# Kernel optimization log

Measured on AMD Instinct MI355X. Metric: run time of the kernel, lower is better.

## Reference

```python
import jax, jax.numpy as jnp
import numpy as np

T_Q, T_K, B, H, V = 32, 48, 64, 1024, 32320
MASK_FILL = -65504.0  # GNMT uses fp16 min


def setup_inputs() -> dict:
    key = jax.random.key(0)
    ks = jax.random.split(key, 12)
    s = 0.02
    inp = {
        "input1": jax.random.normal(ks[0], (T_K, B, H), jnp.float32),
        "input0": jax.random.normal(ks[1], (T_K, B, H), jnp.float32),
        "input2": jax.random.randint(ks[2], (B,), 1, T_K + 1),          # context lengths in [1, T_K]
        "input3": jax.random.randint(ks[3], (T_Q, B), 0, V),            # decoder token ids
        "emb": (jax.random.normal(ks[4], (V, H), jnp.float32) * 0.1).at[0].set(0.0),  # padding_idx=0
        "W_ih": jax.random.normal(ks[5], (4 * H, H), jnp.float32) * s,
        "W_hh": jax.random.normal(ks[6], (4 * H, H), jnp.float32) * s,
        "b_ih": jnp.zeros((4 * H,), jnp.float32),
        "b_hh": jnp.zeros((4 * H,), jnp.float32),
        "W_q": jax.random.normal(ks[7], (H, H), jnp.float32) * s,
        "W_k": jax.random.normal(ks[8], (H, H), jnp.float32) * s,
        "v_att": jax.random.normal(ks[9], (H,), jnp.float32) * s,
        "norm_scalar": jnp.array([1.0 / np.sqrt(H)], jnp.float32),
        "norm_bias": jnp.zeros((H,), jnp.float32),
    }
    return inp


def _lstm(x, W_ih, W_hh, b_ih, b_hh):
    # x: (T, B, In). PyTorch LSTM gate order: i, f, g, o. Zero initial state.
    xp = jnp.einsum('tbi,gi->tbg', x, W_ih) + b_ih + b_hh  # (T, B, 4H)
    Hh = W_hh.shape[1]

    def step(carry, xt):
        h, c = carry
        gates = xt + h @ W_hh.T
        i, f, g, o = jnp.split(gates, 4, axis=-1)
        c = jax.nn.sigmoid(f) * c + jax.nn.sigmoid(i) * jnp.tanh(g)
        h = jax.nn.sigmoid(o) * jnp.tanh(c)
        return (h, c), h

    h0 = jnp.zeros((x.shape[1], Hh), x.dtype)
    _, hs = jax.lax.scan(step, (h0, h0), xp)
    return hs  # (T, B, H)


def _forward(input1, input0, input2, input3, emb, W_ih, W_hh, b_ih, b_hh,
             W_q, W_k, v_att, norm_scalar, norm_bias):
    x = emb[input3]                       # (T_Q, B, H) embedding lookup
    ctx = input0 + input1                 # (T_K, B, H) residual-summed encoder context
    rnn_out = _lstm(x, W_ih, W_hh, b_ih, b_hh)   # (T_Q, B, H)

    # Bahdanau attention (batch_first=False -> transpose to batch-first)
    q = rnn_out.transpose(1, 0, 2)        # (B, T_Q, H)
    keys = ctx.transpose(1, 0, 2)         # (B, T_K, H)
    aq = q @ W_q.T                        # (B, T_Q, H)
    ak = keys @ W_k.T                     # (B, T_K, H)
    v = v_att / jnp.linalg.norm(v_att) * norm_scalar[0]  # normalized attention vector
    sum_qk = aq[:, :, None, :] + ak[:, None, :, :] + norm_bias  # (B, T_Q, T_K, H)
    scores = jnp.einsum('bqkh,h->bqk', jnp.tanh(sum_qk), v)
    pad = jnp.arange(T_K)[None, :] >= input2[:, None]            # (B, T_K), True = pad
    scores = jnp.where(pad[:, None, :], MASK_FILL, scores)
    attn = jax.nn.softmax(scores, axis=-1)
    context = jnp.einsum('bqk,bkh->bqh', attn, keys).transpose(1, 0, 2)  # (T_Q, B, H)
    # dropout p=0 -> identity; returns (rnn_outputs, attn_context) = (out12, out11)
    return rnn_out, context


def reference(input1, input0, input2, input3, emb, W_ih, W_hh, b_ih, b_hh,
              W_q, W_k, v_att, norm_scalar, norm_bias):
    return _forward(input1, input0, input2, input3, emb, W_ih, W_hh, b_ih, b_hh,
                    W_q, W_k, v_att, norm_scalar, norm_bias)
```

## Files before the change

kernel.cpp:

```cpp
#include <hip/hip_runtime.h>
#include <hip/hip_bf16.h>

typedef unsigned short u16;
typedef __attribute__((ext_vector_type(8))) short bf16x8;
typedef __attribute__((ext_vector_type(8))) unsigned short us8;
typedef __attribute__((ext_vector_type(4))) float f32x4;

#define T_Q 32
#define T_K 48
#define NB 64
#define HDIM 1024
#define MASK_FILL -65504.0f
#define LSTM_BLOCKS 64

__device__ __forceinline__ float bf2f(u16 v){
  union { unsigned u; float f; } x; x.u = ((unsigned)v) << 16; return x.f;
}
__device__ __forceinline__ u16 f2bf(float f){
  union { float f; unsigned u; } x; x.f = f;
  return (u16)((x.u + 0x7FFFu + ((x.u >> 16) & 1u)) >> 16);
}
__device__ __forceinline__ float sigm(float x){
  return __builtin_amdgcn_rcpf(1.f + __expf(-x));
}
__device__ __forceinline__ float tanh_f(float x){
  float e = __expf(2.f * x);
  return fmaf(-2.f, __builtin_amdgcn_rcpf(e + 1.f), 1.f);
}

__device__ __forceinline__ void st_b32_cc(u16* a, unsigned v){
  asm volatile("global_store_dword %0, %1, off sc0 sc1" :: "v"(a), "v"(v) : "memory");
}
__device__ __forceinline__ void st_flag(int* a, int v){
  asm volatile("global_store_dword %0, %1, off sc0 sc1" :: "v"(a), "v"(v) : "memory");
}
__device__ __forceinline__ int ld_flag(const int* a){
  int r;
  asm volatile("global_load_dword %0, %1, off sc0 sc1\n\ts_waitcnt vmcnt(0)"
               : "=v"(r) : "v"(a) : "memory");
  return r;
}

#define MFMA16(A,B,C) __builtin_amdgcn_mfma_f32_16x16x32_bf16(A,B,C,0,0,0)


__global__ void conv_f2b(const float* __restrict__ s, u16* __restrict__ d){
  size_t i = ((size_t)blockIdx.x * 256 + threadIdx.x) * 4;
  float4 v = *(const float4*)(s + i);
  ushort4 o; o.x = f2bf(v.x); o.y = f2bf(v.y); o.z = f2bf(v.z); o.w = f2bf(v.w);
  *(ushort4*)(d + i) = o;
}

__global__ void gather_x(const int* __restrict__ tok, const float* __restrict__ emb,
                         u16* __restrict__ x){
  int r = blockIdx.x;
  int token = tok[r];
  float4 v = ((const float4*)(emb + (size_t)token * HDIM))[threadIdx.x];
  ushort4 o; o.x = f2bf(v.x); o.y = f2bf(v.y); o.z = f2bf(v.z); o.w = f2bf(v.w);
  ((ushort4*)(x + (size_t)r * HDIM))[threadIdx.x] = o;
}

__global__ void make_keys(const float* __restrict__ a, const float* __restrict__ b,
                          u16* __restrict__ o){
  size_t i = ((size_t)blockIdx.x * 256 + threadIdx.x) * 4;
  float4 va = *(const float4*)(a + i);
  float4 vb = *(const float4*)(b + i);
  ushort4 vo;
  vo.x = f2bf(va.x + vb.x);
  vo.y = f2bf(va.y + vb.y);
  vo.z = f2bf(va.z + vb.z);
  vo.w = f2bf(va.w + vb.w);
  *(ushort4*)(o + i) = vo;
}

__global__ void prep_small(const float* __restrict__ vatt, const float* __restrict__ ns,
                           const float* __restrict__ nb,
                           float* __restrict__ vhat, float* __restrict__ nbias){
  __shared__ float wred[4];
  int t = threadIdx.x, lane = t & 63, w = t >> 6;
  float vv[4]; float s = 0.f;
  #pragma unroll
  for (int j = 0; j < 4; j++){ vv[j] = vatt[t*4 + j]; s += vv[j]*vv[j]; }
  #pragma unroll
  for (int m = 32; m >= 1; m >>= 1) s += __shfl_xor(s, m);
  if (lane == 0) wred[w] = s;
  __syncthreads();
  float tot = wred[0] + wred[1] + wred[2] + wred[3];
  float scale = ns[0] / sqrtf(tot);
  #pragma unroll
  for (int j = 0; j < 4; j++) vhat[t*4 + j] = vv[j] * scale;
  #pragma unroll
  for (int j = 0; j < 4; j++){ int i = t + 256*j; nbias[i] = nb[i]; }
}

__global__ void prep_bsum(const float* __restrict__ bih, const float* __restrict__ bhh,
                          float* __restrict__ bias_sum){
  int i = blockIdx.x * 256 + threadIdx.x;
  bias_sum[i] = bih[i] + bhh[i];
}


template<int OB>
__global__ __launch_bounds__(256) void gemm_bf16(
  const u16* __restrict__ A, const u16* __restrict__ W,
  const float* __restrict__ bias, void* __restrict__ Cv,
  int M, int N, int K)
{
  __shared__ __align__(16) u16 As[4][66][8];
  __shared__ __align__(16) u16 Bs[4][66][8];
  const int t = threadIdx.x;
  const int m0 = blockIdx.y * 64, n0 = blockIdx.x * 64;
  const int lane = t & 63, w = t >> 6;
  const int wm = (w >> 1) * 32, wn = (w & 1) * 32;
  const int lr = lane & 15, g = lane >> 4;
  const int lrow = t >> 2, lkc = t & 3;
  f32x4 acc00 = {0,0,0,0}, acc01 = {0,0,0,0}, acc10 = {0,0,0,0}, acc11 = {0,0,0,0};
  const u16* aptr = A + (size_t)(m0 + lrow) * K + lkc * 8;
  const u16* wptr = W + (size_t)(n0 + lrow) * K + lkc * 8;
  for (int k0 = 0; k0 < K; k0 += 32){
    *(bf16x8*)(&As[lkc][lrow][0]) = *(const bf16x8*)(aptr + k0);
    *(bf16x8*)(&Bs[lkc][lrow][0]) = *(const bf16x8*)(wptr + k0);
    __syncthreads();
    bf16x8 a0 = *(const bf16x8*)(&As[g][wm      + lr][0]);
    bf16x8 a1 = *(const bf16x8*)(&As[g][wm + 16 + lr][0]);
    bf16x8 b0 = *(const bf16x8*)(&Bs[g][wn      + lr][0]);
    bf16x8 b1 = *(const bf16x8*)(&Bs[g][wn + 16 + lr][0]);
    acc00 = MFMA16(a0, b0, acc00);
    acc01 = MFMA16(a0, b1, acc01);
    acc10 = MFMA16(a1, b0, acc10);
    acc11 = MFMA16(a1, b1, acc11);
    __syncthreads();
  }
  const int rb = m0 + wm + g * 4;
  const int cb = n0 + wn + lr;
  float bv0 = bias ? bias[cb]      : 0.f;
  float bv1 = bias ? bias[cb + 16] : 0.f;
  #pragma unroll
  for (int r = 0; r < 4; r++){
    float v00 = acc00[r] + bv0, v01 = acc01[r] + bv1;
    float v10 = acc10[r] + bv0, v11 = acc11[r] + bv1;
    if (OB){
      u16* C = (u16*)Cv;
      C[(size_t)(rb + r)      * N + cb]      = f2bf(v00);
      C[(size_t)(rb + r)      * N + cb + 16] = f2bf(v01);
      C[(size_t)(rb + 16 + r) * N + cb]      = f2bf(v10);
      C[(size_t)(rb + 16 + r) * N + cb + 16] = f2bf(v11);
    } else {
      float* C = (float*)Cv;
      C[(size_t)(rb + r)      * N + cb]      = v00;
      C[(size_t)(rb + r)      * N + cb + 16] = v01;
      C[(size_t)(rb + 16 + r) * N + cb]      = v10;
      C[(size_t)(rb + 16 + r) * N + cb + 16] = v11;
    }
  }
}


__global__ __launch_bounds__(512, 1) void lstm_persistent(
  const float* __restrict__ Whh, const u16* __restrict__ xp,
  u16* __restrict__ hsteps,
  u16* __restrict__ qbuf, float* __restrict__ out0,
  int* __restrict__ flags)
{
  extern __shared__ char smem[];
  u16*  wlds = (u16*)smem;
  float* gl  = (float*)(smem + 131072);
  volatile int* lds_ready = (volatile int*)(smem + 147456);

  const int tid = threadIdx.x;
  const int c0 = blockIdx.x * 16;
  const int lane = tid & 63, w = tid >> 6;
  const int gate = w & 3, msub = w >> 2;
  const int lr = lane & 15, g = lane >> 4;

  if (tid < 8) lds_ready[tid] = 0;

  #pragma unroll
  for (int i = 0; i < 16; i++){
    int e = (i * 512 + tid) * 8;
    int R = e >> 10, k = e & 1023;
    int gg = R >> 4, rr = R & 15, tt = k >> 5, kk = k & 31;
    const float* src = Whh + (size_t)((gg << 10) + c0 + rr) * 1024 + k;
    float4 v0 = *(const float4*)(src);
    float4 v1 = *(const float4*)(src + 4);
    u16* dst = wlds + (((gg * 32 + tt) * 16 + rr) * 32 + kk);
    ushort4 o0, o1;
    o0.x = f2bf(v0.x); o0.y = f2bf(v0.y); o0.z = f2bf(v0.z); o0.w = f2bf(v0.w);
    o1.x = f2bf(v1.x); o1.y = f2bf(v1.y); o1.z = f2bf(v1.z); o1.w = f2bf(v1.w);
    *(ushort4*)dst = o0; *(ushort4*)(dst + 4) = o1;
  }
  __syncthreads();

  const int pb = (tid * 2) >> 4;
  const int pc = (tid * 2) & 15;
  float c_state0 = 0.f, c_state1 = 0.f;

  const int arow = msub * 32 + lr;
  const int jc = g >> 1;
  const int cc = (g & 1) * 8;

#define SPING(gq) \
  do { while (lds_ready[gq] < step) __builtin_amdgcn_s_sleep(1); \
       asm volatile("" ::: "memory"); } while (0)

#define LOADG(s0, s1, gq) \
  do { const u16* A0_ = pa0 + (gq) * 8192; const u16* A1_ = pa1 + (gq) * 8192; \
       s0[0] = *(const bf16x8*)(A0_);        s1[0] = *(const bf16x8*)(A1_); \
       s0[1] = *(const bf16x8*)(A0_ + 2048); s1[1] = *(const bf16x8*)(A1_ + 2048); \
       s0[2] = *(const bf16x8*)(A0_ + 4096); s1[2] = *(const bf16x8*)(A1_ + 4096); \
       s0[3] = *(const bf16x8*)(A0_ + 6144); s1[3] = *(const bf16x8*)(A1_ + 6144); } while (0)

#define MFMAG(s0, s1, gq) \
  do { const u16* wb_ = wlds + ((size_t)(gate * 32 + (gq) * 4) * 16 + lr) * 32 + g * 8; \
       bf16x8 b0_ = *(const bf16x8*)(wb_); \
       bf16x8 b1_ = *(const bf16x8*)(wb_ + 512); \
       bf16x8 b2_ = *(const bf16x8*)(wb_ + 1024); \
       bf16x8 b3_ = *(const bf16x8*)(wb_ + 1536); \
       acc0 = MFMA16(s0[0], b0_, acc0); acc1 = MFMA16(s1[0], b0_, acc1); \
       acc0 = MFMA16(s0[1], b1_, acc0); acc1 = MFMA16(s1[1], b1_, acc1); \
       acc0 = MFMA16(s0[2], b2_, acc0); acc1 = MFMA16(s1[2], b2_, acc1); \
       acc0 = MFMA16(s0[3], b3_, acc0); acc1 = MFMA16(s1[3], b3_, acc1); } while (0)

  #pragma unroll 1
  for (int step = 0; step < T_Q; step++){
    const u16* xr = xp + ((size_t)(step * NB + pb)) * 4096 + c0 + pc;
    unsigned xw0 = *(const unsigned*)(xr);
    unsigned xw1 = *(const unsigned*)(xr + 1024);
    unsigned xw2 = *(const unsigned*)(xr + 2048);
    unsigned xw3 = *(const unsigned*)(xr + 3072);

    f32x4 acc0 = {0,0,0,0}, acc1 = {0,0,0,0};

    if (step > 0){
      if (w == 0){
        unsigned done = 0;
        const int* fp = flags + lane * 16;
        while (done != 0xFFu){
          int f = ld_flag(fp);
          unsigned long long b = __ballot(f >= step);
          #pragma unroll
          for (int gq = 0; gq < 8; gq++){
            if (((done >> gq) & 1u) == 0 &&
                ((unsigned)(b >> (gq * 8)) & 0xFFu) == 0xFFu){
              if (lane == 0) lds_ready[gq] = step;
              done |= 1u << gq;
            }
          }
          if (done != 0xFFu) __builtin_amdgcn_s_sleep(1);
        }
      }

      const u16* hb  = hsteps + (size_t)(step - 1) * 65536;
      const u16* pa0 = hb + (size_t)jc * 1024 + (size_t)arow * 16 + cc;
      const u16* pa1 = pa0 + 256;

      bf16x8 sA0[4], sA1[4], sB0[4], sB1[4];
      SPING(0); LOADG(sA0, sA1, 0);
      SPING(1); LOADG(sB0, sB1, 1); MFMAG(sA0, sA1, 0);
      SPING(2); LOADG(sA0, sA1, 2); MFMAG(sB0, sB1, 1);
      SPING(3); LOADG(sB0, sB1, 3); MFMAG(sA0, sA1, 2);
      SPING(4); LOADG(sA0, sA1, 4); MFMAG(sB0, sB1, 3);
      SPING(5); LOADG(sB0, sB1, 5); MFMAG(sA0, sA1, 4);
      SPING(6); LOADG(sA0, sA1, 6); MFMAG(sB0, sB1, 5);
      SPING(7); LOADG(sB0, sB1, 7); MFMAG(sA0, sA1, 6);
      MFMAG(sB0, sB1, 7);
    }

    #pragma unroll
    for (int r = 0; r < 4; r++){
      gl[(gate * 64 + msub * 32 +      g * 4 + r) * 16 + lr] = acc0[r];
      gl[(gate * 64 + msub * 32 + 16 + g * 4 + r) * 16 + lr] = acc1[r];
    }
    __syncthreads();

    float hout0, hout1; u16 hb0, hb1;
    {
      float ig = gl[(0 * 64 + pb) * 16 + pc] + bf2f((u16)(xw0 & 0xFFFF));
      float fg = gl[(1 * 64 + pb) * 16 + pc] + bf2f((u16)(xw1 & 0xFFFF));
      float gg = gl[(2 * 64 + pb) * 16 + pc] + bf2f((u16)(xw2 & 0xFFFF));
      float og = gl[(3 * 64 + pb) * 16 + pc] + bf2f((u16)(xw3 & 0xFFFF));
      float cn = sigm(fg) * c_state0 + sigm(ig) * tanh_f(gg);
      c_state0 = cn;
      hout0 = sigm(og) * tanh_f(cn); hb0 = f2bf(hout0);
    }
    {
      float ig = gl[(0 * 64 + pb) * 16 + pc + 1] + bf2f((u16)(xw0 >> 16));
      float fg = gl[(1 * 64 + pb) * 16 + pc + 1] + bf2f((u16)(xw1 >> 16));
      float gg = gl[(2 * 64 + pb) * 16 + pc + 1] + bf2f((u16)(xw2 >> 16));
      float og = gl[(3 * 64 + pb) * 16 + pc + 1] + bf2f((u16)(xw3 >> 16));
      float cn = sigm(fg) * c_state1 + sigm(ig) * tanh_f(gg);
      c_state1 = cn;
      hout1 = sigm(og) * tanh_f(cn); hb1 = f2bf(hout1);
    }

    if (step < T_Q - 1){
      u16* hw = hsteps + (size_t)step * 65536 + (size_t)blockIdx.x * 1024 + pb * 16 + pc;
      unsigned hpack = (unsigned)hb0 | ((unsigned)hb1 << 16);
      st_b32_cc(hw, hpack);
      asm volatile("s_waitcnt vmcnt(0)" ::: "memory");
      __syncthreads();
      if (tid == 0) st_flag(flags + blockIdx.x * 16, step + 1);
    }

    ushort2 hh; hh.x = hb0; hh.y = hb1;
    *(ushort2*)(qbuf + ((size_t)pb * T_Q + step) * HDIM + c0 + pc) = hh;
    float2 ho; ho.x = hout0; ho.y = hout1;
    *(float2*)(out0 + ((size_t)(step * NB + pb)) * HDIM + c0 + pc) = ho;
  }
#undef SPING
#undef LOADG
#undef MFMAG
}


__global__ __launch_bounds__(256) void attn_fused(
  const float* __restrict__ aq, const u16* __restrict__ ak,
  const float* __restrict__ vhat, const u16* __restrict__ keys,
  const int* __restrict__ lens, float* __restrict__ out1)
{
  int b = blockIdx.x >> 5, q = blockIdx.x & 31;
  int t = threadIdx.x, lane = t & 63, w = t >> 6;
  __shared__ float sc[T_K];
  __shared__ float ps[T_K];
  int len = lens[b];
  float aqr[16], vh[16];
  const float* aqp = aq + (size_t)(b * T_Q + q) * HDIM + lane * 16;
  const float* vp  = vhat + lane * 16;
  #pragma unroll
  for (int j = 0; j < 4; j++){
    float4 v0 = ((const float4*)aqp)[j];
    float4 v1 = ((const float4*)vp)[j];
    aqr[j*4+0] = v0.x; aqr[j*4+1] = v0.y; aqr[j*4+2] = v0.z; aqr[j*4+3] = v0.w;
    vh[j*4+0]  = v1.x; vh[j*4+1]  = v1.y; vh[j*4+2]  = v1.z; vh[j*4+3]  = v1.w;
  }

  int kmax = len - w * 12; if (kmax > 12) kmax = 12;
  for (int kk = 0; kk < kmax; kk++){
    int k = w * 12 + kk;
    const u16* akp = ak + (size_t)(k * NB + b) * HDIM + lane * 16;
    us8 a0 = *(const us8*)(akp);
    us8 a1 = *(const us8*)(akp + 8);
    float p = 0.f;
    #pragma unroll
    for (int j = 0; j < 8; j++){
      p += tanh_f(aqr[j]     + bf2f(a0[j])) * vh[j];
      p += tanh_f(aqr[8 + j] + bf2f(a1[j])) * vh[8 + j];
    }
    #pragma unroll
    for (int m = 32; m >= 1; m >>= 1) p += __shfl_xor(p, m);
    if (lane == 0) sc[k] = p;
  }
  __syncthreads();
  float mx = -3.0e38f;
  for (int k = 0; k < len; k++) mx = fmaxf(mx, sc[k]);
  if (t < len) ps[t] = __expf(sc[t] - mx);
  __syncthreads();
  float den = 0.f;
  for (int k = 0; k < len; k++) den += ps[k];
  float rden = __builtin_amdgcn_rcpf(den);

  float c0 = 0.f, c1 = 0.f, c2 = 0.f, c3 = 0.f;
  for (int k = 0; k < len; k++){
    float pk = ps[k];
    ushort4 kv = *(const ushort4*)(keys + (size_t)(k * NB + b) * HDIM + t * 4);
    c0 += pk * bf2f(kv.x); c1 += pk * bf2f(kv.y);
    c2 += pk * bf2f(kv.z); c3 += pk * bf2f(kv.w);
  }
  size_t o = (size_t)(q * NB + b) * HDIM + t * 4;
  out1[o + 0] = c0 * rden;
  out1[o + 1] = c1 * rden;
  out1[o + 2] = c2 * rden;
  out1[o + 3] = c3 * rden;
}


extern "C" void kernel_launch(void* const* d_in, const int* in_sizes, int n_in,
                              void* d_out, int out_size, void* d_ws, size_t ws_size,
                              hipStream_t stream)
{
  const float* in1  = (const float*)d_in[0];
  const float* in0  = (const float*)d_in[1];
  const int*   lens = (const int*)d_in[2];
  const int*   toks = (const int*)d_in[3];
  const float* emb  = (const float*)d_in[4];
  const float* Wih  = (const float*)d_in[5];
  const float* Whh  = (const float*)d_in[6];
  const float* bih  = (const float*)d_in[7];
  const float* bhh  = (const float*)d_in[8];
  const float* Wq   = (const float*)d_in[9];
  const float* Wk   = (const float*)d_in[10];
  const float* vatt = (const float*)d_in[11];
  const float* ns   = (const float*)d_in[12];
  const float* nbb  = (const float*)d_in[13];

  char* p = (char*)d_ws;
  u16* x_bf    = (u16*)p;   p += (size_t)2048 * 1024 * 2;
  u16* keys_bf = (u16*)p;   p += (size_t)3072 * 1024 * 2;
  u16* hsteps  = (u16*)p;   p += (size_t)32 * 65536 * 2;
  u16* qbuf    = (u16*)p;   p += (size_t)2048 * 1024 * 2;
  u16* xp      = (u16*)p;   p += (size_t)2048 * 4096 * 2;
  float* vhat  = (float*)p; p += 1024 * 4;
  float* bsum  = (float*)p; p += 4096 * 4;
  float* nbf   = (float*)p; p += 1024 * 4;
  int* flags   = (int*)p;   p += 4096;
  u16* ak      = (u16*)p;   p += (size_t)3072 * 1024 * 2;
  u16* Wih_bf  = (u16*)p;   p += (size_t)4096 * 1024 * 2;
  u16* Wq_bf   = (u16*)p;   p += (size_t)1024 * 1024 * 2;
  u16* Wk_bf   = (u16*)p;   p += (size_t)1024 * 1024 * 2;
  float* aq    = (float*)xp;

  float* out0 = (float*)d_out;
  float* out1 = out0 + (size_t)T_Q * NB * HDIM;

  hipMemsetAsync(flags, 0, 4096, stream);

  conv_f2b<<<4096, 256, 0, stream>>>(Wih, Wih_bf);
  conv_f2b<<<1024, 256, 0, stream>>>(Wq,  Wq_bf);
  conv_f2b<<<1024, 256, 0, stream>>>(Wk,  Wk_bf);
  gather_x<<<2048, 256, 0, stream>>>(toks, emb, x_bf);
  make_keys<<<3072, 256, 0, stream>>>(in1, in0, keys_bf);
  prep_small<<<1, 256, 0, stream>>>(vatt, ns, nbb, vhat, nbf);
  prep_bsum<<<16, 256, 0, stream>>>(bih, bhh, bsum);

  gemm_bf16<1><<<dim3(64, 32), 256, 0, stream>>>(x_bf, Wih_bf, bsum, xp, 2048, 4096, 1024);
  gemm_bf16<1><<<dim3(16, 48), 256, 0, stream>>>(keys_bf, Wk_bf, nbf, ak, 3072, 1024, 1024);

  lstm_persistent<<<LSTM_BLOCKS, 512, 147488, stream>>>(Whh, xp, hsteps, qbuf, out0, flags);

  gemm_bf16<0><<<dim3(16, 32), 256, 0, stream>>>(qbuf, Wq_bf, nullptr, aq, 2048, 1024, 1024);

  attn_fused<<<2048, 256, 0, stream>>>(aq, ak, vhat, keys_bf, lens, out1);
}
```

Measured before the change: 333.3 us.

## Fuse LSTM input projection into persistent recurrent kernel

```diff
diff --git a/kernel.cpp b/kernel.cpp
--- a/kernel.cpp
+++ b/kernel.cpp
@@ -157,7 +157,8 @@
 
 
 __global__ __launch_bounds__(512, 1) void lstm_persistent(
-  const float* __restrict__ Whh, const u16* __restrict__ xp,
+  const float* __restrict__ Whh, const u16* __restrict__ x_bf,
+  const u16* __restrict__ Wih_bf, const float* __restrict__ bsum,
   u16* __restrict__ hsteps,
   u16* __restrict__ qbuf, float* __restrict__ out0,
   int* __restrict__ flags)
@@ -194,10 +195,17 @@
   const int pb = (tid * 2) >> 4;
   const int pc = (tid * 2) & 15;
   float c_state0 = 0.f, c_state1 = 0.f;
+  float bia[4], bib[4];
+  #pragma unroll
+  for (int g2 = 0; g2 < 4; g2++){
+    bia[g2] = bsum[g2 * 1024 + c0 + pc];
+    bib[g2] = bsum[g2 * 1024 + c0 + pc + 1];
+  }
 
   const int arow = msub * 32 + lr;
   const int jc = g >> 1;
   const int cc = (g & 1) * 8;
+  const u16* wibase = Wih_bf + ((size_t)(gate << 10) + c0 + lr) * 1024 + g * 8;
 
 #define SPING(gq) \
   do { while (lds_ready[gq] < step) __builtin_amdgcn_s_sleep(1); \
@@ -223,11 +231,19 @@
 
   #pragma unroll 1
   for (int step = 0; step < T_Q; step++){
-    const u16* xr = xp + ((size_t)(step * NB + pb)) * 4096 + c0 + pc;
-    unsigned xw0 = *(const unsigned*)(xr);
-    unsigned xw1 = *(const unsigned*)(xr + 1024);
-    unsigned xw2 = *(const unsigned*)(xr + 2048);
-    unsigned xw3 = *(const unsigned*)(xr + 3072);
+    f32x4 ax0 = {0,0,0,0}, ax1 = {0,0,0,0};
+    {
+      const u16* xb0 = x_bf + ((size_t)(step * NB) + arow) * 1024 + g * 8;
+      const u16* xb1 = xb0 + (size_t)16 * 1024;
+      #pragma unroll 4
+      for (int t = 0; t < 32; t++){
+        bf16x8 xa = *(const bf16x8*)(xb0 + t * 32);
+        bf16x8 xc = *(const bf16x8*)(xb1 + t * 32);
+        bf16x8 bw = *(const bf16x8*)(wibase + t * 32);
+        ax0 = MFMA16(xa, bw, ax0);
+        ax1 = MFMA16(xc, bw, ax1);
+      }
+    }
 
     f32x4 acc0 = {0,0,0,0}, acc1 = {0,0,0,0};
 
@@ -268,26 +284,26 @@
 
     #pragma unroll
     for (int r = 0; r < 4; r++){
-      gl[(gate * 64 + msub * 32 +      g * 4 + r) * 16 + lr] = acc0[r];
-      gl[(gate * 64 + msub * 32 + 16 + g * 4 + r) * 16 + lr] = acc1[r];
+      gl[(gate * 64 + msub * 32 +      g * 4 + r) * 16 + lr] = acc0[r] + ax0[r];
+      gl[(gate * 64 + msub * 32 + 16 + g * 4 + r) * 16 + lr] = acc1[r] + ax1[r];
     }
     __syncthreads();
 
     float hout0, hout1; u16 hb0, hb1;
     {
-      float ig = gl[(0 * 64 + pb) * 16 + pc] + bf2f((u16)(xw0 & 0xFFFF));
-      float fg = gl[(1 * 64 + pb) * 16 + pc] + bf2f((u16)(xw1 & 0xFFFF));
-      float gg = gl[(2 * 64 + pb) * 16 + pc] + bf2f((u16)(xw2 & 0xFFFF));
-      float og = gl[(3 * 64 + pb) * 16 + pc] + bf2f((u16)(xw3 & 0xFFFF));
+      float ig = gl[(0 * 64 + pb) * 16 + pc] + bia[0];
+      float fg = gl[(1 * 64 + pb) * 16 + pc] + bia[1];
+      float gg = gl[(2 * 64 + pb) * 16 + pc] + bia[2];
+      float og = gl[(3 * 64 + pb) * 16 + pc] + bia[3];
       float cn = sigm(fg) * c_state0 + sigm(ig) * tanh_f(gg);
       c_state0 = cn;
       hout0 = sigm(og) * tanh_f(cn); hb0 = f2bf(hout0);
     }
     {
-      float ig = gl[(0 * 64 + pb) * 16 + pc + 1] + bf2f((u16)(xw0 >> 16));
-      float fg = gl[(1 * 64 + pb) * 16 + pc + 1] + bf2f((u16)(xw1 >> 16));
-      float gg = gl[(2 * 64 + pb) * 16 + pc + 1] + bf2f((u16)(xw2 >> 16));
-      float og = gl[(3 * 64 + pb) * 16 + pc + 1] + bf2f((u16)(xw3 >> 16));
+      float ig = gl[(0 * 64 + pb) * 16 + pc + 1] + bib[0];
+      float fg = gl[(1 * 64 + pb) * 16 + pc + 1] + bib[1];
+      float gg = gl[(2 * 64 + pb) * 16 + pc + 1] + bib[2];
+      float og = gl[(3 * 64 + pb) * 16 + pc + 1] + bib[3];
       float cn = sigm(fg) * c_state1 + sigm(ig) * tanh_f(gg);
       c_state1 = cn;
       hout1 = sigm(og) * tanh_f(cn); hb1 = f2bf(hout1);
@@ -398,7 +414,7 @@
   u16* keys_bf = (u16*)p;   p += (size_t)3072 * 1024 * 2;
   u16* hsteps  = (u16*)p;   p += (size_t)32 * 65536 * 2;
   u16* qbuf    = (u16*)p;   p += (size_t)2048 * 1024 * 2;
-  u16* xp      = (u16*)p;   p += (size_t)2048 * 4096 * 2;
+  float* aq    = (float*)p; p += (size_t)2048 * 1024 * 4;
   float* vhat  = (float*)p; p += 1024 * 4;
   float* bsum  = (float*)p; p += 4096 * 4;
   float* nbf   = (float*)p; p += 1024 * 4;
@@ -407,7 +423,6 @@
   u16* Wih_bf  = (u16*)p;   p += (size_t)4096 * 1024 * 2;
   u16* Wq_bf   = (u16*)p;   p += (size_t)1024 * 1024 * 2;
   u16* Wk_bf   = (u16*)p;   p += (size_t)1024 * 1024 * 2;
-  float* aq    = (float*)xp;
 
   float* out0 = (float*)d_out;
   float* out1 = out0 + (size_t)T_Q * NB * HDIM;
@@ -422,10 +437,10 @@
   prep_small<<<1, 256, 0, stream>>>(vatt, ns, nbb, vhat, nbf);
   prep_bsum<<<16, 256, 0, stream>>>(bih, bhh, bsum);
 
-  gemm_bf16<1><<<dim3(64, 32), 256, 0, stream>>>(x_bf, Wih_bf, bsum, xp, 2048, 4096, 1024);
   gemm_bf16<1><<<dim3(16, 48), 256, 0, stream>>>(keys_bf, Wk_bf, nbf, ak, 3072, 1024, 1024);
 
-  lstm_persistent<<<LSTM_BLOCKS, 512, 147488, stream>>>(Whh, xp, hsteps, qbuf, out0, flags);
+  lstm_persistent<<<LSTM_BLOCKS, 512, 147488, stream>>>(Whh, x_bf, Wih_bf, bsum,
+                                                        hsteps, qbuf, out0, flags);
 
   gemm_bf16<0><<<dim3(16, 32), 256, 0, stream>>>(qbuf, Wq_bf, nullptr, aq, 2048, 1024, 1024);
 
```

Result: slower. 941.5 us (median of 2 runs) (+182.5%).

## Fuse input-projection and key GEMMs into a persistent LSTM megakernel with flag pipelining

Applied to the files above, without the earlier changes.

```diff
diff --git a/kernel.cpp b/kernel.cpp
--- a/kernel.cpp
+++ b/kernel.cpp
@@ -30,6 +30,10 @@
 
 __device__ __forceinline__ void st_b32_cc(u16* a, unsigned v){
   asm volatile("global_store_dword %0, %1, off sc0 sc1" :: "v"(a), "v"(v) : "memory");
+}
+__device__ __forceinline__ void st_b16_cc(u16* a, u16 v){
+  unsigned vv = v;
+  asm volatile("global_store_short %0, %1, off sc0 sc1" :: "v"(a), "v"(vv) : "memory");
 }
 __device__ __forceinline__ void st_flag(int* a, int v){
   asm volatile("global_store_dword %0, %1, off sc0 sc1" :: "v"(a), "v"(v) : "memory");
@@ -155,23 +159,106 @@
   }
 }
 
-
-__global__ __launch_bounds__(512, 1) void lstm_persistent(
-  const float* __restrict__ Whh, const u16* __restrict__ xp,
-  u16* __restrict__ hsteps,
-  u16* __restrict__ qbuf, float* __restrict__ out0,
+__device__ __forceinline__ void load_w_lds(const float* W, int row0, u16* wlds, int tid){
+  #pragma unroll
+  for (int i = 0; i < 16; i++){
+    int e = (i * 512 + tid) * 8;
+    int R = e >> 10, k = e & 1023;
+    int gg = R >> 4, rr = R & 15, tt = k >> 5, kk = k & 31;
+    const float* src = W + (size_t)(row0 + gg * 16 + rr) * 1024 + k;
+    float4 v0 = *(const float4*)(src);
+    float4 v1 = *(const float4*)(src + 4);
+    u16* dst = wlds + (((gg * 32 + tt) * 16 + rr) * 32 + kk);
+    ushort4 o0, o1;
+    o0.x = f2bf(v0.x); o0.y = f2bf(v0.y); o0.z = f2bf(v0.z); o0.w = f2bf(v0.w);
+    o1.x = f2bf(v1.x); o1.y = f2bf(v1.y); o1.z = f2bf(v1.z); o1.w = f2bf(v1.w);
+    *(ushort4*)dst = o0; *(ushort4*)(dst + 4) = o1;
+  }
+}
+
+
+__global__ __launch_bounds__(512, 1) void mega(
+  const float* __restrict__ Whh, const float* __restrict__ Wih,
+  const float* __restrict__ Wk,
+  const u16* __restrict__ x_bf, const u16* __restrict__ keys_bf,
+  const float* __restrict__ bsum, const float* __restrict__ nbf,
+  u16* __restrict__ xp, u16* __restrict__ akbuf,
+  u16* __restrict__ hsteps, u16* __restrict__ qbuf, float* __restrict__ out0,
   int* __restrict__ flags)
 {
   extern __shared__ char smem[];
+  const int bid = blockIdx.x;
+  const int tid = threadIdx.x;
+  const int lane = tid & 63, w = tid >> 6;
+  const int lr = lane & 15, g = lane >> 4;
+
+  if (bid >= 64){
+    u16* wlds = (u16*)smem;
+    const int wm = (w >> 2) * 32, wn = (w & 3) * 16, gg = wn >> 4;
+
+    if (bid < 128){
+      const int j = bid - 64;
+      load_w_lds(Wih, j * 64, wlds, tid);
+      __syncthreads();
+      const float bv = bsum[j * 64 + wn + lr];
+      #pragma unroll 1
+      for (int step = 0; step < T_Q; step++){
+        f32x4 acc0 = {0,0,0,0}, acc1 = {0,0,0,0};
+        const u16* a0p = x_bf + ((size_t)(step * NB) + wm + lr) * 1024 + g * 8;
+        const u16* a1p = a0p + (size_t)16 * 1024;
+        #pragma unroll 4
+        for (int t = 0; t < 32; t++){
+          bf16x8 a0 = *(const bf16x8*)(a0p + t * 32);
+          bf16x8 a1 = *(const bf16x8*)(a1p + t * 32);
+          bf16x8 b  = *(const bf16x8*)(wlds + ((size_t)(gg * 32 + t) * 16 + lr) * 32 + g * 8);
+          acc0 = MFMA16(a0, b, acc0);
+          acc1 = MFMA16(a1, b, acc1);
+        }
+        #pragma unroll
+        for (int r = 0; r < 4; r++){
+          int row0 = wm + g * 4 + r;
+          st_b16_cc(xp + ((size_t)(step * NB) + row0) * 4096 + j * 64 + wn + lr,
+                    f2bf(acc0[r] + bv));
+          st_b16_cc(xp + ((size_t)(step * NB) + row0 + 16) * 4096 + j * 64 + wn + lr,
+                    f2bf(acc1[r] + bv));
+        }
+        asm volatile("s_waitcnt vmcnt(0)" ::: "memory");
+        __syncthreads();
+        if (tid == 0) st_flag(flags + (64 + j) * 16, step + 1);
+      }
+    } else {
+      const int t2 = bid - 128;
+      const int bx = t2 & 15, by = t2 >> 4;
+      load_w_lds(Wk, bx * 64, wlds, tid);
+      __syncthreads();
+      const float bv = nbf[bx * 64 + wn + lr];
+      f32x4 acc0 = {0,0,0,0}, acc1 = {0,0,0,0};
+      const u16* a0p = keys_bf + ((size_t)(by * 64) + wm + lr) * 1024 + g * 8;
+      const u16* a1p = a0p + (size_t)16 * 1024;
+      #pragma unroll 4
+      for (int t = 0; t < 32; t++){
+        bf16x8 a0 = *(const bf16x8*)(a0p + t * 32);
+        bf16x8 a1 = *(const bf16x8*)(a1p + t * 32);
+        bf16x8 b  = *(const bf16x8*)(wlds + ((size_t)(gg * 32 + t) * 16 + lr) * 32 + g * 8);
+        acc0 = MFMA16(a0, b, acc0);
+        acc1 = MFMA16(a1, b, acc1);
+      }
+      #pragma unroll
+      for (int r = 0; r < 4; r++){
+        int row0 = by * 64 + wm + g * 4 + r;
+        akbuf[(size_t)row0 * 1024 + bx * 64 + wn + lr]        = f2bf(acc0[r] + bv);
+        akbuf[(size_t)(row0 + 16) * 1024 + bx * 64 + wn + lr] = f2bf(acc1[r] + bv);
+      }
+    }
+    return;
+  }
+
   u16*  wlds = (u16*)smem;
   float* gl  = (float*)(smem + 131072);
   volatile int* lds_ready = (volatile int*)(smem + 147456);
 
-  const int tid = threadIdx.x;
-  const int c0 = blockIdx.x * 16;
-  const int lane = tid & 63, w = tid >> 6;
+  const int c0 = bid * 16;
   const int gate = w & 3, msub = w >> 2;
-  const int lr = lane & 15, g = lane >> 4;
 
   if (tid < 8) lds_ready[tid] = 0;
 
@@ -198,6 +285,7 @@
   const int arow = msub * 32 + lr;
   const int jc = g >> 1;
   const int cc = (g & 1) * 8;
+  const int* fxp = flags + (64 + (lane & 3) * 16 + (bid >> 2)) * 16;
 
 #define SPING(gq) \
   do { while (lds_ready[gq] < step) __builtin_amdgcn_s_sleep(1); \
@@ -223,21 +311,28 @@
 
   #pragma unroll 1
   for (int step = 0; step < T_Q; step++){
-    const u16* xr = xp + ((size_t)(step * NB + pb)) * 4096 + c0 + pc;
-    unsigned xw0 = *(const unsigned*)(xr);
-    unsigned xw1 = *(const unsigned*)(xr + 1024);
-    unsigned xw2 = *(const unsigned*)(xr + 2048);
-    unsigned xw3 = *(const unsigned*)(xr + 3072);
-
     f32x4 acc0 = {0,0,0,0}, acc1 = {0,0,0,0};
 
-    if (step > 0){
+    if (step == 0){
+      if (w == 0){
+        for (;;){
+          int f2 = ld_flag(fxp);
+          if (__ballot(lane < 4 ? (f2 >= 1) : 1) == ~0ull) break;
+          __builtin_amdgcn_s_sleep(1);
+        }
+      }
+    } else {
       if (w == 0){
         unsigned done = 0;
+        bool xpok = false;
         const int* fp = flags + lane * 16;
-        while (done != 0xFFu){
+        while (done != 0xFFu || !xpok){
           int f = ld_flag(fp);
           unsigned long long b = __ballot(f >= step);
+          if (!xpok){
+            int f2 = ld_flag(fxp);
+            xpok = (__ballot(lane < 4 ? (f2 >= step + 1) : 1) == ~0ull);
+          }
           #pragma unroll
           for (int gq = 0; gq < 8; gq++){
             if (((done >> gq) & 1u) == 0 &&
@@ -246,7 +341,7 @@
               done |= 1u << gq;
             }
           }
-          if (done != 0xFFu) __builtin_amdgcn_s_sleep(1);
+          if (done != 0xFFu || !xpok) __builtin_amdgcn_s_sleep(1);
         }
       }
 
@@ -273,33 +368,38 @@
     }
     __syncthreads();
 
+    const u16* xr = xp + ((size_t)(step * NB + pb)) * 4096 + c0 + pc;
+    unsigned xw0 = *(const unsigned*)(xr);
+    unsigned xw1 = *(const unsigned*)(xr + 1024);
+    unsigned xw2 = *(const unsigned*)(xr + 2048);
+    unsigned xw3 = *(const unsigned*)(xr + 3072);
+
     float hout0, hout1; u16 hb0, hb1;
     {
       float ig = gl[(0 * 64 + pb) * 16 + pc] + bf2f((u16)(xw0 & 0xFFFF));
       float fg = gl[(1 * 64 + pb) * 16 + pc] + bf2f((u16)(xw1 & 0xFFFF));
-      float gg = gl[(2 * 64 + pb) * 16 + pc] + bf2f((u16)(xw2 & 0xFFFF));
+      float gg2 = gl[(2 * 64 + pb) * 16 + pc] + bf2f((u16)(xw2 & 0xFFFF));
       float og = gl[(3 * 64 + pb) * 16 + pc] + bf2f((u16)(xw3 & 0xFFFF));
-      float cn = sigm(fg) * c_state0 + sigm(ig) * tanh_f(gg);
+      float cn = sigm(fg) * c_state0 + sigm(ig) * tanh_f(gg2);
       c_state0 = cn;
       hout0 = sigm(og) * tanh_f(cn); hb0 = f2bf(hout0);
     }
     {
       float ig = gl[(0 * 64 + pb) * 16 + pc + 1] + bf2f((u16)(xw0 >> 16));
       float fg = gl[(1 * 64 + pb) * 16 + pc + 1] + bf2f((u16)(xw1 >> 16));
-      float gg = gl[(2 * 64 + pb) * 16 + pc + 1] + bf2f((u16)(xw2 >> 16));
+      float gg2 = gl[(2 * 64 + pb) * 16 + pc + 1] + bf2f((u16)(xw2 >> 16));
       float og = gl[(3 * 64 + pb) * 16 + pc + 1] + bf2f((u16)(xw3 >> 16));
-      float cn = sigm(fg) * c_state1 + sigm(ig) * tanh_f(gg);
+      float cn = sigm(fg) * c_state1 + sigm(ig) * tanh_f(gg2);
       c_state1 = cn;
       hout1 = sigm(og) * tanh_f(cn); hb1 = f2bf(hout1);
     }
 
     if (step < T_Q - 1){
-      u16* hw = hsteps + (size_t)step * 65536 + (size_t)blockIdx.x * 1024 + pb * 16 + pc;
-      unsigned hpack = (unsigned)hb0 | ((unsigned)hb1 << 16);
-      st_b32_cc(hw, hpack);
+      u16* hw = hsteps + (size_t)step * 65536 + (size_t)bid * 1024 + pb * 16 + pc;
+      st_b32_cc(hw, (unsigned)hb0 | ((unsigned)hb1 << 16));
       asm volatile("s_waitcnt vmcnt(0)" ::: "memory");
       __syncthreads();
-      if (tid == 0) st_flag(flags + blockIdx.x * 16, step + 1);
+      if (tid == 0) st_flag(flags + bid * 16, step + 1);
     }
 
     ushort2 hh; hh.x = hb0; hh.y = hb1;
@@ -402,30 +502,24 @@
   float* vhat  = (float*)p; p += 1024 * 4;
   float* bsum  = (float*)p; p += 4096 * 4;
   float* nbf   = (float*)p; p += 1024 * 4;
-  int* flags   = (int*)p;   p += 4096;
+  int* flags   = (int*)p;   p += 8192;
   u16* ak      = (u16*)p;   p += (size_t)3072 * 1024 * 2;
-  u16* Wih_bf  = (u16*)p;   p += (size_t)4096 * 1024 * 2;
   u16* Wq_bf   = (u16*)p;   p += (size_t)1024 * 1024 * 2;
-  u16* Wk_bf   = (u16*)p;   p += (size_t)1024 * 1024 * 2;
   float* aq    = (float*)xp;
 
   float* out0 = (float*)d_out;
   float* out1 = out0 + (size_t)T_Q * NB * HDIM;
 
-  hipMemsetAsync(flags, 0, 4096, stream);
-
-  conv_f2b<<<4096, 256, 0, stream>>>(Wih, Wih_bf);
-  conv_f2b<<<1024, 256, 0, stream>>>(Wq,  Wq_bf);
-  conv_f2b<<<1024, 256, 0, stream>>>(Wk,  Wk_bf);
+  hipMemsetAsync(flags, 0, 8192, stream);
+
+  conv_f2b<<<1024, 256, 0, stream>>>(Wq, Wq_bf);
   gather_x<<<2048, 256, 0, stream>>>(toks, emb, x_bf);
   make_keys<<<3072, 256, 0, stream>>>(in1, in0, keys_bf);
   prep_small<<<1, 256, 0, stream>>>(vatt, ns, nbb, vhat, nbf);
   prep_bsum<<<16, 256, 0, stream>>>(bih, bhh, bsum);
 
-  gemm_bf16<1><<<dim3(64, 32), 256, 0, stream>>>(x_bf, Wih_bf, bsum, xp, 2048, 4096, 1024);
-  gemm_bf16<1><<<dim3(16, 48), 256, 0, stream>>>(keys_bf, Wk_bf, nbf, ak, 3072, 1024, 1024);
-
-  lstm_persistent<<<LSTM_BLOCKS, 512, 147488, stream>>>(Whh, xp, hsteps, qbuf, out0, flags);
+  mega<<<896, 512, 147488, stream>>>(Whh, Wih, Wk, x_bf, keys_bf, bsum, nbf,
+                                     xp, ak, hsteps, qbuf, out0, flags);
 
   gemm_bf16<0><<<dim3(16, 32), 256, 0, stream>>>(qbuf, Wq_bf, nullptr, aq, 2048, 1024, 1024);
 
```

Result: slower. 557.9 us (+67.4%).
